# Kernel optimization log

Measured on AMD Instinct MI355X. Metric: run time of the kernel, lower is better.

Reference implementation:

```python
import jax, jax.numpy as jnp
import numpy as np

DIM = 256        # word / relation / entity-type embedding dim
STATEDIM = 256   # agent state dim
VOCAB = 100000
REL_COUNT = 25
T = 128          # sentence length


def _lstm(wvs, Wih, Whh, bih, bhh, reverse):
    # PyTorch LSTMCell gate order: i, f, g, o
    def step(carry, x):
        h, c = carry
        g = x @ Wih.T + bih + h @ Whh.T + bhh
        i, f, gg, o = jnp.split(g, 4)
        c = jax.nn.sigmoid(f) * c + jax.nn.sigmoid(i) * jnp.tanh(gg)
        h = jax.nn.sigmoid(o) * jnp.tanh(c)
        return (h, c), h
    init = (jnp.zeros((DIM,), jnp.float32), jnp.zeros((DIM,), jnp.float32))
    _, hs = jax.lax.scan(step, init, wvs, reverse=reverse)
    return hs


def setup_inputs() -> dict:
    key = jax.random.key(0)
    ks = jax.random.split(key, 32)
    def p(i, shape, scale=0.05):
        return (jax.random.normal(ks[i], shape) * scale).astype(jnp.float32)
    return {
        "text": jax.random.randint(ks[0], (T,), 0, VOCAB, dtype=jnp.int32),
        "wordvector": p(1, (VOCAB, DIM)),
        "relvec": p(2, (REL_COUNT + 1, DIM)),
        "entvec": p(3, (7, DIM)),
        "WihL": p(4, (4 * DIM, DIM)), "WhhL": p(5, (4 * DIM, DIM)),
        "bihL": p(6, (4 * DIM,)), "bhhL": p(7, (4 * DIM,)),
        "WihR": p(8, (4 * DIM, DIM)), "WhhR": p(9, (4 * DIM, DIM)),
        "bihR": p(10, (4 * DIM,)), "bhhR": p(11, (4 * DIM,)),
        "Wt": p(12, (STATEDIM, 3 * DIM + STATEDIM)), "bt": p(13, (STATEDIM,)),
        "Wp": p(14, (REL_COUNT + 1, STATEDIM)), "bp": p(15, (REL_COUNT + 1,)),
        "Wb": p(16, (STATEDIM, 3 * DIM + 2 * STATEDIM)), "bb": p(17, (STATEDIM,)),
        "Wpl": p(18, (REL_COUNT, 7, STATEDIM)), "bpl": p(19, (REL_COUNT, 7)),
        "Wtt": p(20, (STATEDIM, STATEDIM)), "btt": p(21, (STATEDIM,)),
        "Wtb": p(22, (STATEDIM, STATEDIM)), "btb": p(23, (STATEDIM,)),
        "Wbt": p(24, (STATEDIM, STATEDIM)), "bbt": p(25, (STATEDIM,)),
    }


def reference(text, wordvector, relvec, entvec, WihL, WhhL, bihL, bhhL,
              WihR, WhhR, bihR, bhhR, Wt, bt, Wp, bp, Wb, bb, Wpl, bpl,
              Wtt, btt, Wtb, btb, Wbt, bbt):
    # mode = "test_NER": deterministic argmax sampling, dropout disabled.
    wvs = wordvector[text]                               # [T, DIM]
    front = _lstm(wvs, WihL, WhhL, bihL, bhhL, False)    # [T, DIM]
    back = _lstm(wvs, WihR, WhhR, bihR, bhhR, True)      # [T, DIM]
    wordin = jnp.concatenate([front, back], axis=1)      # [T, 2*DIM]

    def bot_rollout(rel_idx, target, memb0):
        Wr, br = Wpl[rel_idx], bpl[rel_idx]              # per-relation head
        def stepb(carry, w):
            memb, ab = carry
            inpb = jnp.concatenate([w, entvec[ab], memb, target])
            outb = jnp.tanh(inpb @ Wb.T + bb)            # dropout off (test)
            probb = jax.nn.softmax(outb @ Wr.T + br)
            ab2 = jnp.argmax(probb).astype(jnp.int32)
            return (outb, ab2), (ab2, probb[ab2])
        (membf, _), (acts, aps) = jax.lax.scan(
            stepb, (memb0, jnp.zeros((), jnp.int32)), wordin)
        return membf, acts, aps

    def top_step(carry, w):
        mem, rel_action = carry
        inp = jnp.concatenate([w, relvec[rel_action], mem])
        outp = jnp.tanh(inp @ Wt.T + bt)                 # dropout off (test)
        prob = jax.nn.softmax(outp @ Wp.T + bp)
        action = jnp.argmax(prob).astype(jnp.int32)
        actprob = prob[action]
        do_ner = action > 0
        rel_next = jnp.where(do_ner, action, rel_action)
        rel_idx = jnp.maximum(action, 1) - 1
        target = outp @ Wtt.T + btt
        memb0 = outp @ Wtb.T + btb
        membf, acts, aps = bot_rollout(rel_idx, target, memb0)
        mem_after = membf @ Wbt.T + bbt
        mem_next = jnp.where(do_ner, mem_after, outp)
        acts = jnp.where(do_ner, acts, 0)
        aps = jnp.where(do_ner, aps, 0.0)
        return (mem_next, rel_next), (action, actprob, acts, aps)

    init = (jnp.zeros((STATEDIM,), jnp.float32), jnp.zeros((), jnp.int32))
    _, (top_actions, top_actprobs, bot_actions, bot_actprobs) = jax.lax.scan(
        top_step, init, wordin)
    # bot rows where no NER sub-rollout fired are zero-filled (orig: empty lists)
    return top_actions, top_actprobs, bot_actions, bot_actprobs
```

## Files before the change

### kernel.cpp

```cpp
#include <hip/hip_runtime.h>
#include <float.h>

constexpr int SEQ  = 128;
constexpr int D    = 256;
constexpr int G    = 1024;
constexpr int NREL = 26;
constexpr int NENT = 7;

typedef float v2f __attribute__((ext_vector_type(2)));

__global__ void k_trans(const float* __restrict__ in, float* __restrict__ out,
                        int rows, int cols, int in_stride, int in_off)
{
    int idx = blockIdx.x * 256 + threadIdx.x;
    if (idx >= rows * cols) return;
    int i = idx % rows;
    int k = idx / rows;
    out[idx] = in[(size_t)i * in_stride + in_off + k];
}

__global__ __launch_bounds__(1024) void k_xg(
    const int* __restrict__ text, const float* __restrict__ wv,
    const float* __restrict__ Wih, const float* __restrict__ bih,
    const float* __restrict__ bhh, float* __restrict__ xg)
{
    int t = blockIdx.x, j = threadIdx.x;
    const float* x  = wv + (size_t)text[t] * D;
    const float* wr = Wih + (size_t)j * D;
    float acc = bih[j] + bhh[j];
    for (int k = 0; k < D; ++k) acc += x[k] * wr[k];
    xg[t * G + j] = acc;
}

__global__ __launch_bounds__(1024) void k_lstm(
    const float* __restrict__ xgF, const float* __restrict__ xgB,
    const float* __restrict__ WHTF, const float* __restrict__ WHTB,
    float* __restrict__ wordin)
{
    int dir = blockIdx.x;
    const float* xg  = dir ? xgB  : xgF;
    const float* WHT = dir ? WHTB : WHTF;
    __shared__ float h[D], c[D], g[G];
    int j = threadIdx.x;
    if (j < D) { h[j] = 0.f; c[j] = 0.f; }
    __syncthreads();
    for (int s = 0; s < SEQ; ++s) {
        int t = dir ? (SEQ - 1 - s) : s;
        float acc = xg[t * G + j];
        for (int k = 0; k < D; ++k) acc += WHT[k * G + j] * h[k];
        g[j] = acc;
        __syncthreads();
        if (j < D) {
            float si = 1.f / (1.f + expf(-g[j]));
            float sf = 1.f / (1.f + expf(-g[D + j]));
            float gg = tanhf(g[2 * D + j]);
            float so = 1.f / (1.f + expf(-g[3 * D + j]));
            float cn = sf * c[j] + si * gg;
            float hn = so * tanhf(cn);
            c[j] = cn; h[j] = hn;
            wordin[t * (2 * D) + dir * D + j] = hn;
        }
        __syncthreads();
    }
}

__global__ __launch_bounds__(256) void k_prep2(
    const float* __restrict__ wordin,
    const float* __restrict__ WTWT, const float* __restrict__ WBWT,
    const float* __restrict__ WTRT, const float* __restrict__ WBET,
    const float* __restrict__ relvec, const float* __restrict__ entvec,
    const float* __restrict__ btv, const float* __restrict__ bbv,
    float* __restrict__ TW, float* __restrict__ BW,
    float* __restrict__ RV, float* __restrict__ EV)
{
    int b = blockIdx.x, i = threadIdx.x;
    if (b < SEQ) {
        const float* w = wordin + b * (2 * D);
        float a1 = btv[i], a2 = bbv[i];
        for (int j = 0; j < 2 * D; ++j) {
            float wv = w[j];
            a1 += wv * WTWT[j * D + i];
            a2 += wv * WBWT[j * D + i];
        }
        TW[b * D + i] = a1;
        BW[b * D + i] = a2;
    } else if (b < SEQ + NREL) {
        int r = b - SEQ;
        const float* x = relvec + r * D;
        float a = 0.f;
        for (int k = 0; k < D; ++k) a += x[k] * WTRT[k * D + i];
        RV[r * D + i] = a;
    } else {
        int e = b - SEQ - NREL;
        const float* x = entvec + e * D;
        float a = 0.f;
        for (int k = 0; k < D; ++k) a += x[k] * WBET[k * D + i];
        EV[e * D + i] = a;
    }
}

__global__ __launch_bounds__(256) void k_m1(
    const float* __restrict__ WBGT, const float* __restrict__ Wtt,
    float* __restrict__ M1T)
{
    int j = blockIdx.x, i = threadIdx.x;
    float a = 0.f;
    for (int k = 0; k < D; ++k) a = fmaf(WBGT[k * D + i], Wtt[k * D + j], a);
    M1T[j * D + i] = a;
}

__global__ __launch_bounds__(256) void k_c1(
    const float* __restrict__ WBGT, const float* __restrict__ btt,
    float* __restrict__ c1)
{
    int i = threadIdx.x;
    float a = 0.f;
    for (int k = 0; k < D; ++k) a = fmaf(WBGT[k * D + i], btt[k], a);
    c1[i] = a;
}

__global__ __launch_bounds__(256) void k_pack4(
    const float* __restrict__ Wb, float* __restrict__ WB4)
{
    int e = blockIdx.x * 256 + threadIdx.x;
    int tid = e >> 6, kk = e & 63;
    int q = tid >> 8, i = tid & 255;
    WB4[e] = Wb[(size_t)i * (5 * D) + 3 * D + q * 64 + kk];
}

__device__ inline float mv_q(const float* __restrict__ Wcol,
                             const float* __restrict__ x)
{
    float a0 = 0.f, a1 = 0.f, a2 = 0.f, a3 = 0.f;
    #pragma unroll
    for (int kk = 0; kk < 64; kk += 4) {
        a0 = fmaf(Wcol[(kk + 0) * D], x[kk + 0], a0);
        a1 = fmaf(Wcol[(kk + 1) * D], x[kk + 1], a1);
        a2 = fmaf(Wcol[(kk + 2) * D], x[kk + 2], a2);
        a3 = fmaf(Wcol[(kk + 3) * D], x[kk + 3], a3);
    }
    return (a0 + a1) + (a2 + a3);
}

template<int W>
__device__ inline void grp_smax(float lv, int n, int lane, int& am, float& pm)
{
    float mx = lv;
    #pragma unroll
    for (int off = W / 2; off; off >>= 1) mx = fmaxf(mx, __shfl_xor(mx, off));
    float e  = (lane < n) ? expf(lv - mx) : 0.f;
    float se = e;
    #pragma unroll
    for (int off = W / 2; off; off >>= 1) se += __shfl_xor(se, off);
    float p  = (lane < n) ? (e / se) : -1.f;
    float q  = p;
    #pragma unroll
    for (int off = W / 2; off; off >>= 1) q = fmaxf(q, __shfl_xor(q, off));
    unsigned long long mask = __ballot(p == q);
    am = __ffsll((long long)mask) - 1;
    pm = q;
}

__global__ __launch_bounds__(1024, 4)
void k_main3(
    const float* __restrict__ TW,   const float* __restrict__ BW,
    const float* __restrict__ RV,   const float* __restrict__ EV,
    const float* __restrict__ WTMT, const float* __restrict__ WTBT,
    const float* __restrict__ WBTT, const float* __restrict__ M1T,
    const float* __restrict__ c1v,  const float* __restrict__ WB4,
    const float* __restrict__ Wp,   const float* __restrict__ bp,
    const float* __restrict__ Wpl,  const float* __restrict__ bpl,
    const float* __restrict__ btb,  const float* __restrict__ bbt,
    float* __restrict__ out)
{
    const int tid  = threadIdx.x;
    const int lane = tid & 63;
    const int lwv  = (tid >> 6) & 3;
    const int q    = tid >> 8;
    const int i    = tid & 255;
    const bool lower = (tid < 256);

    __shared__ __align__(16) float xbuf[2][D];
    __shared__ __align__(16) float psA[4][D], psB[4][D];
    __shared__ __align__(16) float mem[D], outv[D];
    __shared__ __align__(16) float WrSh[NENT * D];
    __shared__ float lpart[4][32];
    __shared__ float brSh[8];

    v2f w2[32];
    {
        const float4* src = reinterpret_cast<const float4*>(WB4) + tid * 16;
        #pragma unroll
        for (int k4 = 0; k4 < 16; ++k4) {
            float4 v = src[k4];
            w2[2 * k4 + 0] = (v2f){v.x, v.y};
            w2[2 * k4 + 1] = (v2f){v.z, v.w};
        }
    }
    #pragma unroll
    for (int k2 = 0; k2 < 32; ++k2) {
        double dp = __builtin_bit_cast(double, w2[k2]);
        asm volatile("" : "+v"(dp));
        w2[k2] = __builtin_bit_cast(v2f, dp);
    }
    float ev0 = 0.f, ev1 = 0.f, ev2 = 0.f, ev3 = 0.f,
          ev4 = 0.f, ev5 = 0.f, ev6 = 0.f;
    if (lower) {
        ev0 = EV[0 * D + i]; ev1 = EV[1 * D + i]; ev2 = EV[2 * D + i];
        ev3 = EV[3 * D + i]; ev4 = EV[4 * D + i]; ev5 = EV[5 * D + i];
        ev6 = EV[6 * D + i];
        mem[i] = 0.f;
    }
    __syncthreads();

    const float* WTMq = WTMT + (size_t)q * 64 * D + i;
    const float* WTBq = WTBT + (size_t)q * 64 * D + i;
    const float* WBTq = WBTT + (size_t)q * 64 * D + i;
    const float* M1q  = M1T  + (size_t)q * 64 * D + i;

    int rel = 0;

    for (int t = 0; t < SEQ; ++t) {
        psA[q][i] = mv_q(WTMq, mem + q * 64);
        __syncthreads();
        if (lower) {
            float tot = psA[0][i] + psA[1][i] + psA[2][i] + psA[3][i] +
                        TW[t * D + i] + RV[rel * D + i];
            float outp = tanhf(tot);
            outv[i] = outp;
            #pragma unroll
            for (int r = 0; r < NREL; ++r) {
                float pp = outp * Wp[r * D + i];
                #pragma unroll
                for (int off = 32; off; off >>= 1) pp += __shfl_xor(pp, off);
                if (lane == 0) lpart[lwv][r] = pp;
            }
        }
        __syncthreads();
        float lv = -FLT_MAX;
        if (lane < NREL)
            lv = lpart[0][lane] + lpart[1][lane] + lpart[2][lane] +
                 lpart[3][lane] + bp[lane];
        int am; float pm;
        grp_smax<32>(lv, NREL, lane, am, pm);
        if (tid == 0) { out[t] = (float)am; out[SEQ + t] = pm; }
        const int action = am;

        if (action > 0) {
            rel = action;
            psA[q][i] = mv_q(WTBq, outv + q * 64);
            psB[q][i] = mv_q(M1q,  outv + q * 64);
            const size_t wbase = (size_t)(action - 1) * NENT * D;
            for (int k = tid; k < NENT * D; k += 1024) WrSh[k] = Wpl[wbase + k];
            if (tid < NENT) brSh[tid] = bpl[(action - 1) * NENT + tid];
            __syncthreads();
            float btm = 0.f, bwc = 0.f;
            if (lower) {
                xbuf[0][i] = psA[0][i] + psA[1][i] + psA[2][i] + psA[3][i] +
                             btb[i];
                btm = psB[0][i] + psB[1][i] + psB[2][i] + psB[3][i] + c1v[i];
                bwc = BW[i];
            }
            __syncthreads();

            int p = 0, ab = 0;
            for (int s = 0; s < SEQ; ++s) {
                const float4* xb =
                    reinterpret_cast<const float4*>(xbuf[p] + q * 64);
                v2f A0 = {0.f, 0.f}, A1 = {0.f, 0.f},
                    A2 = {0.f, 0.f}, A3 = {0.f, 0.f};
                #pragma unroll
                for (int k4 = 0; k4 < 16; k4 += 4) {
                    float4 x0 = xb[k4], x1 = xb[k4 + 1],
                           x2 = xb[k4 + 2], x3 = xb[k4 + 3];
                    A0 = __builtin_elementwise_fma(w2[2 * k4 + 0], (v2f){x0.x, x0.y}, A0);
                    A0 = __builtin_elementwise_fma(w2[2 * k4 + 1], (v2f){x0.z, x0.w}, A0);
                    A1 = __builtin_elementwise_fma(w2[2 * k4 + 2], (v2f){x1.x, x1.y}, A1);
                    A1 = __builtin_elementwise_fma(w2[2 * k4 + 3], (v2f){x1.z, x1.w}, A1);
                    A2 = __builtin_elementwise_fma(w2[2 * k4 + 4], (v2f){x2.x, x2.y}, A2);
                    A2 = __builtin_elementwise_fma(w2[2 * k4 + 5], (v2f){x2.z, x2.w}, A2);
                    A3 = __builtin_elementwise_fma(w2[2 * k4 + 6], (v2f){x3.x, x3.y}, A3);
                    A3 = __builtin_elementwise_fma(w2[2 * k4 + 7], (v2f){x3.z, x3.w}, A3);
                }
                v2f AS = (A0 + A1) + (A2 + A3);
                float ms = AS.x + AS.y;
                psA[q][i] = ms;
                __syncthreads();
                if (lower) {
                    float ev = (ab == 0) ? ev0 : (ab == 1) ? ev1 :
                               (ab == 2) ? ev2 : (ab == 3) ? ev3 :
                               (ab == 4) ? ev4 : (ab == 5) ? ev5 : ev6;
                    float tot = ms + psA[1][i] + psA[2][i] + psA[3][i] +
                                bwc + ev + btm;
                    float ob = tanhf(tot);
                    xbuf[p ^ 1][i] = ob;
                    #pragma unroll
                    for (int r = 0; r < NENT; ++r) {
                        float pp = ob * WrSh[r * D + i];
                        #pragma unroll
                        for (int off = 32; off; off >>= 1)
                            pp += __shfl_xor(pp, off);
                        if (lane == 0) lpart[lwv][r] = pp;
                    }
                    int sn = (s + 1 < SEQ) ? s + 1 : s;
                    bwc = BW[sn * D + i];
                }
                __syncthreads();
                float lv2 = -FLT_MAX;
                if (lane < NENT)
                    lv2 = lpart[0][lane] + lpart[1][lane] + lpart[2][lane] +
                          lpart[3][lane] + brSh[lane];
                int am2; float pm2;
                grp_smax<8>(lv2, NENT, lane, am2, pm2);
                if (tid == 0) {
                    out[2 * SEQ + t * SEQ + s] = (float)am2;
                    out[2 * SEQ + SEQ * SEQ + t * SEQ + s] = pm2;
                }
                ab = am2;
                p ^= 1;
            }
            psA[q][i] = mv_q(WBTq, xbuf[p] + q * 64);
            __syncthreads();
            if (lower)
                mem[i] = psA[0][i] + psA[1][i] + psA[2][i] + psA[3][i] +
                         bbt[i];
            __syncthreads();
        } else {
            if (lower) mem[i] = outv[i];
            if (tid < SEQ) {
                out[2 * SEQ + t * SEQ + tid] = 0.f;
                out[2 * SEQ + SEQ * SEQ + t * SEQ + tid] = 0.f;
            }
            __syncthreads();
        }
    }
}

extern "C" void kernel_launch(void* const* d_in, const int* in_sizes, int n_in,
                              void* d_out, int out_size, void* d_ws, size_t ws_size,
                              hipStream_t stream)
{
    (void)in_sizes; (void)n_in; (void)out_size; (void)ws_size;
    const int*   text       = (const int*)  d_in[0];
    const float* wordvector = (const float*)d_in[1];
    const float* relvec     = (const float*)d_in[2];
    const float* entvec     = (const float*)d_in[3];
    const float* WihL = (const float*)d_in[4];  const float* WhhL = (const float*)d_in[5];
    const float* bihL = (const float*)d_in[6];  const float* bhhL = (const float*)d_in[7];
    const float* WihR = (const float*)d_in[8];  const float* WhhR = (const float*)d_in[9];
    const float* bihR = (const float*)d_in[10]; const float* bhhR = (const float*)d_in[11];
    const float* Wt   = (const float*)d_in[12]; const float* bt   = (const float*)d_in[13];
    const float* Wp   = (const float*)d_in[14]; const float* bp   = (const float*)d_in[15];
    const float* Wb   = (const float*)d_in[16]; const float* bb   = (const float*)d_in[17];
    const float* Wpl  = (const float*)d_in[18]; const float* bpl  = (const float*)d_in[19];
    const float* Wtt  = (const float*)d_in[20]; const float* btt  = (const float*)d_in[21];
    const float* Wtb  = (const float*)d_in[22]; const float* btb  = (const float*)d_in[23];
    const float* Wbt  = (const float*)d_in[24]; const float* bbt  = (const float*)d_in[25];

    float* ws = (float*)d_ws;
    size_t o = 0;
    auto take = [&](size_t n) { float* p = ws + o; o += n; return p; };
    float* XGF    = take(SEQ * G);
    float* XGB    = take(SEQ * G);
    float* WHLT   = take(D * G);
    float* WHRT   = take(D * G);
    float* WORDIN = take(SEQ * 2 * D);
    float* TW     = take(SEQ * D);
    float* BW     = take(SEQ * D);
    float* RVb    = take(NREL * D);
    float* EVb    = take(NENT * D);
    float* WTWT   = take(2 * D * D);
    float* WTRT   = take(D * D);
    float* WTMT   = take(D * D);
    float* WBWT   = take(2 * D * D);
    float* WBET   = take(D * D);
    float* WBGT   = take(D * D);
    float* WTBT   = take(D * D);
    float* WBTT   = take(D * D);
    float* M1T    = take(D * D);
    float* C1     = take(D);
    float* WB4    = take(1024 * 64);

    auto tr = [&](const float* in, float* outp, int rows, int cols, int stride, int off) {
        int n = rows * cols;
        k_trans<<<(n + 255) / 256, 256, 0, stream>>>(in, outp, rows, cols, stride, off);
    };
    tr(WhhL, WHLT, G, D, D, 0);
    tr(WhhR, WHRT, G, D, D, 0);
    tr(Wt,  WTWT, D, 2 * D, G, 0);
    tr(Wt,  WTRT, D, D, G, 512);
    tr(Wt,  WTMT, D, D, G, 768);
    tr(Wb,  WBWT, D, 2 * D, 5 * D, 0);
    tr(Wb,  WBET, D, D, 5 * D, 512);
    tr(Wb,  WBGT, D, D, 5 * D, 1024);
    tr(Wtb, WTBT, D, D, D, 0);
    tr(Wbt, WBTT, D, D, D, 0);

    k_m1<<<D, D, 0, stream>>>(WBGT, Wtt, M1T);
    k_c1<<<1, D, 0, stream>>>(WBGT, btt, C1);
    k_pack4<<<256, 256, 0, stream>>>(Wb, WB4);

    k_xg<<<SEQ, 1024, 0, stream>>>(text, wordvector, WihL, bihL, bhhL, XGF);
    k_xg<<<SEQ, 1024, 0, stream>>>(text, wordvector, WihR, bihR, bhhR, XGB);
    k_lstm<<<2, 1024, 0, stream>>>(XGF, XGB, WHLT, WHRT, WORDIN);
    k_prep2<<<SEQ + NREL + NENT, 256, 0, stream>>>(WORDIN, WTWT, WBWT, WTRT, WBET,
                                                   relvec, entvec, bt, bb,
                                                   TW, BW, RVb, EVb);
    k_main3<<<1, 1024, 0, stream>>>(TW, BW, RVb, EVb, WTMT, WTBT, WBTT, M1T, C1,
                                    WB4, Wp, bp, Wpl, bpl, btb, bbt,
                                    (float*)d_out);
}
```

Baseline: 57.85 ms.

## Halve main kernel to 512 threads, split bottom weights between registers and LDS

The serial main kernel now runs with 512 threads instead of 1024. Each thread covers 128 of the 256 reduction inputs: half of its bottom-recurrence weight column stays in registers and the other half is pre-packed into a 128KB LDS array. The aim is to cut barrier cost and the cross-wave partial-sum reduction (two partials instead of four) on the latency-bound inner loop. The cost is twice as many FMAs per thread plus LDS reads on every step, and the large LDS footprint.

```diff
diff --git a/kernel.cpp b/kernel.cpp
--- a/kernel.cpp
+++ b/kernel.cpp
@@ -119,21 +119,32 @@
     c1[i] = a;
 }
 
-__global__ __launch_bounds__(256) void k_pack4(
-    const float* __restrict__ Wb, float* __restrict__ WB4)
+__global__ __launch_bounds__(256) void k_pack5r(
+    const float* __restrict__ Wb, float* __restrict__ WB5R)
 {
     int e = blockIdx.x * 256 + threadIdx.x;
     int tid = e >> 6, kk = e & 63;
-    int q = tid >> 8, i = tid & 255;
-    WB4[e] = Wb[(size_t)i * (5 * D) + 3 * D + q * 64 + kk];
-}
-
-__device__ inline float mv_q(const float* __restrict__ Wcol,
-                             const float* __restrict__ x)
+    int h = tid >> 8, i = tid & 255;
+    WB5R[e] = Wb[(size_t)i * (5 * D) + 3 * D + h * 128 + kk];
+}
+
+__global__ __launch_bounds__(256) void k_pack5l(
+    const float* __restrict__ Wb, float* __restrict__ WB5L)
+{
+    int f = blockIdx.x * 256 + threadIdx.x;
+    int f4 = f >> 2, c = f & 3;
+    int l = f4 & 63, j = (f4 >> 6) & 15, wv = f4 >> 10;
+    int tid = wv * 64 + l;
+    int h = tid >> 8, i = tid & 255;
+    WB5L[f] = Wb[(size_t)i * (5 * D) + 3 * D + h * 128 + 64 + j * 4 + c];
+}
+
+__device__ inline float mv_half(const float* __restrict__ Wcol,
+                                const float* __restrict__ x)
 {
     float a0 = 0.f, a1 = 0.f, a2 = 0.f, a3 = 0.f;
     #pragma unroll
-    for (int kk = 0; kk < 64; kk += 4) {
+    for (int kk = 0; kk < 128; kk += 4) {
         a0 = fmaf(Wcol[(kk + 0) * D], x[kk + 0], a0);
         a1 = fmaf(Wcol[(kk + 1) * D], x[kk + 1], a1);
         a2 = fmaf(Wcol[(kk + 2) * D], x[kk + 2], a2);
@@ -161,13 +172,14 @@
     pm = q;
 }
 
-__global__ __launch_bounds__(1024, 4)
-void k_main3(
+__global__ __launch_bounds__(512)
+void k_main5(
     const float* __restrict__ TW,   const float* __restrict__ BW,
     const float* __restrict__ RV,   const float* __restrict__ EV,
     const float* __restrict__ WTMT, const float* __restrict__ WTBT,
     const float* __restrict__ WBTT, const float* __restrict__ M1T,
-    const float* __restrict__ c1v,  const float* __restrict__ WB4,
+    const float* __restrict__ c1v,  const float* __restrict__ WB5R,
+    const float* __restrict__ WB5L,
     const float* __restrict__ Wp,   const float* __restrict__ bp,
     const float* __restrict__ Wpl,  const float* __restrict__ bpl,
     const float* __restrict__ btb,  const float* __restrict__ bbt,
@@ -175,21 +187,30 @@
 {
     const int tid  = threadIdx.x;
     const int lane = tid & 63;
-    const int lwv  = (tid >> 6) & 3;
-    const int q    = tid >> 8;
+    const int wv8  = tid >> 6;
+    const int lwv  = wv8 & 3;
+    const int h    = tid >> 8;
     const int i    = tid & 255;
     const bool lower = (tid < 256);
 
+    __shared__ __align__(16) float wlds[512 * 64];
     __shared__ __align__(16) float xbuf[2][D];
-    __shared__ __align__(16) float psA[4][D], psB[4][D];
+    __shared__ __align__(16) float psA[2][D], psB[2][D];
     __shared__ __align__(16) float mem[D], outv[D];
     __shared__ __align__(16) float WrSh[NENT * D];
     __shared__ float lpart[4][32];
     __shared__ float brSh[8];
 
+    {
+        const float4* g4 = reinterpret_cast<const float4*>(WB5L);
+        float4* w4 = reinterpret_cast<float4*>(wlds);
+        #pragma unroll
+        for (int it = 0; it < 16; ++it) w4[tid + it * 512] = g4[tid + it * 512];
+    }
+
     v2f w2[32];
     {
-        const float4* src = reinterpret_cast<const float4*>(WB4) + tid * 16;
+        const float4* src = reinterpret_cast<const float4*>(WB5R) + tid * 16;
         #pragma unroll
         for (int k4 = 0; k4 < 16; ++k4) {
             float4 v = src[k4];
@@ -203,6 +224,7 @@
         asm volatile("" : "+v"(dp));
         w2[k2] = __builtin_bit_cast(v2f, dp);
     }
+
     float ev0 = 0.f, ev1 = 0.f, ev2 = 0.f, ev3 = 0.f,
           ev4 = 0.f, ev5 = 0.f, ev6 = 0.f;
     if (lower) {
@@ -213,22 +235,25 @@
     }
     __syncthreads();
 
-    const float* WTMq = WTMT + (size_t)q * 64 * D + i;
-    const float* WTBq = WTBT + (size_t)q * 64 * D + i;
-    const float* WBTq = WBTT + (size_t)q * 64 * D + i;
-    const float* M1q  = M1T  + (size_t)q * 64 * D + i;
+    const float4* wbase =
+        reinterpret_cast<const float4*>(wlds) + (size_t)wv8 * (16 * 64) + lane;
+
+    const float* WTMh = WTMT + (size_t)h * 128 * D + i;
+    const float* WTBh = WTBT + (size_t)h * 128 * D + i;
+    const float* WBTh = WBTT + (size_t)h * 128 * D + i;
+    const float* M1h  = M1T  + (size_t)h * 128 * D + i;
 
     int rel = 0;
 
     for (int t = 0; t < SEQ; ++t) {
-        psA[q][i] = mv_q(WTMq, mem + q * 64);
+        psA[h][i] = mv_half(WTMh, mem + h * 128);
         __syncthreads();
         if (lower) {
-            float tot = psA[0][i] + psA[1][i] + psA[2][i] + psA[3][i] +
+            float tot = psA[0][i] + psA[1][i] +
                         TW[t * D + i] + RV[rel * D + i];
             float outp = tanhf(tot);
             outv[i] = outp;
-            #pragma unroll
+            #pragma unroll 2
             for (int r = 0; r < NREL; ++r) {
                 float pp = outp * Wp[r * D + i];
                 #pragma unroll
@@ -248,17 +273,16 @@
 
         if (action > 0) {
             rel = action;
-            psA[q][i] = mv_q(WTBq, outv + q * 64);
-            psB[q][i] = mv_q(M1q,  outv + q * 64);
-            const size_t wbase = (size_t)(action - 1) * NENT * D;
-            for (int k = tid; k < NENT * D; k += 1024) WrSh[k] = Wpl[wbase + k];
+            psA[h][i] = mv_half(WTBh, outv + h * 128);
+            psB[h][i] = mv_half(M1h,  outv + h * 128);
+            const size_t wbaseW = (size_t)(action - 1) * NENT * D;
+            for (int k = tid; k < NENT * D; k += 512) WrSh[k] = Wpl[wbaseW + k];
             if (tid < NENT) brSh[tid] = bpl[(action - 1) * NENT + tid];
             __syncthreads();
             float btm = 0.f, bwc = 0.f;
             if (lower) {
-                xbuf[0][i] = psA[0][i] + psA[1][i] + psA[2][i] + psA[3][i] +
-                             btb[i];
-                btm = psB[0][i] + psB[1][i] + psB[2][i] + psB[3][i] + c1v[i];
+                xbuf[0][i] = psA[0][i] + psA[1][i] + btb[i];
+                btm = psB[0][i] + psB[1][i] + c1v[i];
                 bwc = BW[i];
             }
             __syncthreads();
@@ -266,7 +290,7 @@
             int p = 0, ab = 0;
             for (int s = 0; s < SEQ; ++s) {
                 const float4* xb =
-                    reinterpret_cast<const float4*>(xbuf[p] + q * 64);
+                    reinterpret_cast<const float4*>(xbuf[p] + h * 128);
                 v2f A0 = {0.f, 0.f}, A1 = {0.f, 0.f},
                     A2 = {0.f, 0.f}, A3 = {0.f, 0.f};
                 #pragma unroll
@@ -282,16 +306,30 @@
                     A3 = __builtin_elementwise_fma(w2[2 * k4 + 6], (v2f){x3.x, x3.y}, A3);
                     A3 = __builtin_elementwise_fma(w2[2 * k4 + 7], (v2f){x3.z, x3.w}, A3);
                 }
+                #pragma unroll
+                for (int j = 0; j < 16; j += 4) {
+                    float4 wa = wbase[(j + 0) * 64], wb_ = wbase[(j + 1) * 64],
+                           wc = wbase[(j + 2) * 64], wd  = wbase[(j + 3) * 64];
+                    float4 xa = xb[16 + j],     xv = xb[17 + j],
+                           xc = xb[18 + j],     xd = xb[19 + j];
+                    A0 = __builtin_elementwise_fma((v2f){wa.x, wa.y}, (v2f){xa.x, xa.y}, A0);
+                    A0 = __builtin_elementwise_fma((v2f){wa.z, wa.w}, (v2f){xa.z, xa.w}, A0);
+                    A1 = __builtin_elementwise_fma((v2f){wb_.x, wb_.y}, (v2f){xv.x, xv.y}, A1);
+                    A1 = __builtin_elementwise_fma((v2f){wb_.z, wb_.w}, (v2f){xv.z, xv.w}, A1);
+                    A2 = __builtin_elementwise_fma((v2f){wc.x, wc.y}, (v2f){xc.x, xc.y}, A2);
+                    A2 = __builtin_elementwise_fma((v2f){wc.z, wc.w}, (v2f){xc.z, xc.w}, A2);
+                    A3 = __builtin_elementwise_fma((v2f){wd.x, wd.y}, (v2f){xd.x, xd.y}, A3);
+                    A3 = __builtin_elementwise_fma((v2f){wd.z, wd.w}, (v2f){xd.z, xd.w}, A3);
+                }
                 v2f AS = (A0 + A1) + (A2 + A3);
                 float ms = AS.x + AS.y;
-                psA[q][i] = ms;
+                psA[h][i] = ms;
                 __syncthreads();
                 if (lower) {
                     float ev = (ab == 0) ? ev0 : (ab == 1) ? ev1 :
                                (ab == 2) ? ev2 : (ab == 3) ? ev3 :
                                (ab == 4) ? ev4 : (ab == 5) ? ev5 : ev6;
-                    float tot = ms + psA[1][i] + psA[2][i] + psA[3][i] +
-                                bwc + ev + btm;
+                    float tot = ms + psA[1][i] + bwc + ev + btm;
                     float ob = tanhf(tot);
                     xbuf[p ^ 1][i] = ob;
                     #pragma unroll
@@ -319,11 +357,9 @@
                 ab = am2;
                 p ^= 1;
             }
-            psA[q][i] = mv_q(WBTq, xbuf[p] + q * 64);
+            psA[h][i] = mv_half(WBTh, xbuf[p] + h * 128);
             __syncthreads();
-            if (lower)
-                mem[i] = psA[0][i] + psA[1][i] + psA[2][i] + psA[3][i] +
-                         bbt[i];
+            if (lower) mem[i] = psA[0][i] + psA[1][i] + bbt[i];
             __syncthreads();
         } else {
             if (lower) mem[i] = outv[i];
@@ -379,7 +415,8 @@
     float* WBTT   = take(D * D);
     float* M1T    = take(D * D);
     float* C1     = take(D);
-    float* WB4    = take(1024 * 64);
+    float* WB5R   = take(512 * 64);
+    float* WB5L   = take(512 * 64);
 
     auto tr = [&](const float* in, float* outp, int rows, int cols, int stride, int off) {
         int n = rows * cols;
@@ -398,7 +435,8 @@
 
     k_m1<<<D, D, 0, stream>>>(WBGT, Wtt, M1T);
     k_c1<<<1, D, 0, stream>>>(WBGT, btt, C1);
-    k_pack4<<<256, 256, 0, stream>>>(Wb, WB4);
+    k_pack5r<<<128, 256, 0, stream>>>(Wb, WB5R);
+    k_pack5l<<<128, 256, 0, stream>>>(Wb, WB5L);
 
     k_xg<<<SEQ, 1024, 0, stream>>>(text, wordvector, WihL, bihL, bhhL, XGF);
     k_xg<<<SEQ, 1024, 0, stream>>>(text, wordvector, WihR, bihR, bhhR, XGB);
@@ -406,7 +444,7 @@
     k_prep2<<<SEQ + NREL + NENT, 256, 0, stream>>>(WORDIN, WTWT, WBWT, WTRT, WBET,
                                                    relvec, entvec, bt, bb,
                                                    TW, BW, RVb, EVb);
-    k_main3<<<1, 1024, 0, stream>>>(TW, BW, RVb, EVb, WTMT, WTBT, WBTT, M1T, C1,
-                                    WB4, Wp, bp, Wpl, bpl, btb, bbt,
-                                    (float*)d_out);
-}
+    k_main5<<<1, 512, 0, stream>>>(TW, BW, RVb, EVb, WTMT, WTBT, WBTT, M1T, C1,
+                                   WB5R, WB5L, Wp, bp, Wpl, bpl, btb, bbt,
+                                   (float*)d_out);
+}
```

Measured after the change: 62.46 ms. +8.0%, slower.
